# Kernel tuning notes

Hardware: AMD Instinct MI355X
Metric: run time of the kernel (lower is better)

Reference implementation:

```python
import jax, jax.numpy as jnp
import numpy as np

DIM = 512
KEY_DIM = 32
NUM_HEADS = 8
ATTN_RATIO = 4
RES = 1024
B = 16
NH_KD = KEY_DIM * NUM_HEADS          # 256
D = ATTN_RATIO * KEY_DIM             # 128
DH = D * NUM_HEADS                   # 1024
H_QKV = DH + 2 * NH_KD               # 1536
EPS = 1e-5
SCALE = KEY_DIM ** -0.5


def bn(y, g, b, m, v):
    # eval-mode BatchNorm1d over channel dim of [B, C, L]
    inv = g / jnp.sqrt(v + EPS)
    return (y - m[None, :, None]) * inv[None, :, None] + b[None, :, None]


def setup_inputs() -> dict:
    key = jax.random.key(0)
    ks = jax.random.split(key, 16)
    x = jax.random.normal(ks[0], (B, DIM, RES), dtype=jnp.float32)
    w_qkv = jax.random.normal(ks[1], (H_QKV, DIM), dtype=jnp.float32) * 0.02
    qkv_g = jnp.ones((H_QKV,), jnp.float32)
    qkv_b = jnp.zeros((H_QKV,), jnp.float32)
    qkv_m = jax.random.normal(ks[2], (H_QKV,), jnp.float32) * 0.1
    qkv_v = jax.random.uniform(ks[3], (H_QKV,), jnp.float32) + 0.5
    w_dw = jax.random.normal(ks[4], (NH_KD, 1, 3), jnp.float32) * 0.1
    dw_g = jnp.ones((NH_KD,), jnp.float32)
    dw_b = jnp.zeros((NH_KD,), jnp.float32)
    dw_m = jax.random.normal(ks[5], (NH_KD,), jnp.float32) * 0.1
    dw_v = jax.random.uniform(ks[6], (NH_KD,), jnp.float32) + 0.5
    w_proj = jax.random.normal(ks[7], (DIM, DH), jnp.float32) * 0.02
    proj_g = jnp.ones((DIM,), jnp.float32)  # bn_weight_init=0 in source, use 1 for nontrivial output
    proj_b = jnp.zeros((DIM,), jnp.float32)
    proj_m = jax.random.normal(ks[8], (DIM,), jnp.float32) * 0.1
    proj_v = jax.random.uniform(ks[9], (DIM,), jnp.float32) + 0.5
    attention_biases = jax.random.normal(ks[10], (NUM_HEADS, RES), jnp.float32) * 0.02
    pts = jnp.arange(RES)
    bias_idxs = jnp.abs(pts[:, None] - pts[None, :]).astype(jnp.int32)  # [N, N]
    return dict(x=x, w_qkv=w_qkv, qkv_g=qkv_g, qkv_b=qkv_b, qkv_m=qkv_m, qkv_v=qkv_v,
                w_dw=w_dw, dw_g=dw_g, dw_b=dw_b, dw_m=dw_m, dw_v=dw_v,
                w_proj=w_proj, proj_g=proj_g, proj_b=proj_b, proj_m=proj_m, proj_v=proj_v,
                attention_biases=attention_biases, bias_idxs=bias_idxs)


def reference(x, w_qkv, qkv_g, qkv_b, qkv_m, qkv_v,
              w_dw, dw_g, dw_b, dw_m, dw_v,
              w_proj, proj_g, proj_b, proj_m, proj_v,
              attention_biases, bias_idxs):
    Bsz, _, L = x.shape
    # qkv: conv1x1 + BN
    qkv = bn(jnp.einsum('bcl,oc->bol', x, w_qkv), qkv_g, qkv_b, qkv_m, qkv_v)
    q = qkv[:, :NH_KD]
    k = qkv[:, NH_KD:2 * NH_KD]
    v = qkv[:, 2 * NH_KD:]
    # depthwise conv k=3 pad=1 on q, then BN
    q = jax.lax.conv_general_dilated(q, w_dw, window_strides=(1,), padding=((1, 1),),
                                     dimension_numbers=('NCH', 'OIH', 'NCH'),
                                     feature_group_count=NH_KD)
    q = bn(q, dw_g, dw_b, dw_m, dw_v)
    q = q.reshape(Bsz, NUM_HEADS, KEY_DIM, L)
    k = k.reshape(Bsz, NUM_HEADS, KEY_DIM, L)
    v = v.reshape(Bsz, NUM_HEADS, D, L)
    ab = attention_biases[:, bias_idxs]  # [H, N, N]
    attn = jnp.einsum('bhdn,bhdm->bhnm', q, k) * SCALE + ab[None]
    attn = jax.nn.softmax(attn, axis=-1)
    out = jnp.einsum('bhdm,bhnm->bhdn', v, attn).reshape(Bsz, DH, L)
    # proj: ReLU -> conv1x1 -> BN
    out = jax.nn.relu(out)
    out = bn(jnp.einsum('bcl,oc->bol', out, w_proj), proj_g, proj_b, proj_m, proj_v)
    return out
```

## Files before the change

### kernel.cpp

```cpp
#include <hip/hip_runtime.h>
#include <stdint.h>

#define DEV __device__ __forceinline__

typedef unsigned short u16;
typedef __bf16 bf16x8 __attribute__((ext_vector_type(8)));
typedef float floatx4 __attribute__((ext_vector_type(4)));
typedef unsigned short u16x4 __attribute__((ext_vector_type(4)));
typedef unsigned short u16x8 __attribute__((ext_vector_type(8)));
typedef short s16x4 __attribute__((ext_vector_type(4)));


DEV u16 f2bf(float x) {
  union { float f; uint32_t u; } v; v.f = x;
  uint32_t r = v.u + 0x7FFFu + ((v.u >> 16) & 1u);
  return (u16)(r >> 16);
}
DEV float bf2f(u16 x) {
  union { uint32_t u; float f; } v; v.u = ((uint32_t)x) << 16;
  return v.f;
}
DEV float loadf(const void* p, int i, int bf) {
  return bf ? bf2f(((const u16*)p)[i]) : ((const float*)p)[i];
}
DEV u16 fastbf(float x) {
  union { float f; uint32_t u; } v; v.f = x;
  return (u16)((v.u + 0x8000u) >> 16);
}
DEV bf16x8 u2b(u16x8 v) {
  union { u16x8 u; bf16x8 b; } x; x.u = v; return x.b;
}

DEV floatx4 mfma16(bf16x8 a, bf16x8 b, floatx4 c) {
  return __builtin_amdgcn_mfma_f32_16x16x32_bf16(a, b, c, 0, 0, 0);
}

DEV void gl_lds16(const void* g, void* l) {
  __builtin_amdgcn_global_load_lds(
      (const __attribute__((address_space(1))) void*)g,
      (__attribute__((address_space(3))) void*)l, 16, 0, 0);
}

__global__ void sniff(const uint32_t* __restrict__ x, int* __restrict__ flag) {
  int lane = threadIdx.x & 63;
  int hits = 0;
#pragma unroll
  for (int i = 0; i < 4; ++i) {
    uint32_t u = x[lane * 4 + i];
    int e = (u >> 7) & 0xFF;
    hits += (e >= 100 && e <= 140) ? 1 : 0;
  }
  unsigned long long m = __ballot(hits >= 3);
  if (lane == 0) *flag = (__popcll(m) >= 40) ? 1 : 0;
}

__global__ __launch_bounds__(256) void cvt_all(
    const void* __restrict__ a, const void* __restrict__ b,
    const void* __restrict__ c, const void* __restrict__ d,
    u16* __restrict__ oa, u16* __restrict__ ob, u16* __restrict__ oc,
    u16* __restrict__ od, const int* __restrict__ flag) {
  int i = blockIdx.x * 256 + threadIdx.x;
  int bf = *flag;
  if (i < 786432) {
    oa[i] = bf ? ((const u16*)a)[i] : f2bf(((const float*)a)[i]);
  } else if (i < 1310720) {
    int j = i - 786432;
    ob[j] = bf ? ((const u16*)b)[j] : f2bf(((const float*)b)[j]);
  } else if (i < 1311488) {
    int j = i - 1310720;
    oc[j] = bf ? ((const u16*)c)[j] : f2bf(((const float*)c)[j]);
  } else if (i < 1319680) {
    int j = i - 1311488;
    od[j] = bf ? ((const u16*)d)[j] : f2bf(((const float*)d)[j]);
  }
}

__global__ __launch_bounds__(256) void prep_params(
    const void* qg, const void* qb, const void* qm, const void* qv,
    const void* dg, const void* db, const void* dm, const void* dv,
    const void* pg, const void* pb, const void* pm, const void* pv,
    float* scl, float* shf, const int* __restrict__ flag) {
  int i = blockIdx.x * 256 + threadIdx.x;
  if (i >= 2304) return;
  int bf = *flag;
  float g, b, m, v;
  if (i < 1536)      { g = loadf(qg, i, bf); b = loadf(qb, i, bf); m = loadf(qm, i, bf); v = loadf(qv, i, bf); }
  else if (i < 1792) { int j = i - 1536; g = loadf(dg, j, bf); b = loadf(db, j, bf); m = loadf(dm, j, bf); v = loadf(dv, j, bf); }
  else               { int j = i - 1792; g = loadf(pg, j, bf); b = loadf(pb, j, bf); m = loadf(pm, j, bf); v = loadf(pv, j, bf); }
  float s = g / sqrtf(v + 1e-5f);
  scl[i] = s;
  shf[i] = b - m * s;
}

__global__ __launch_bounds__(256) void transpose_x(const void* __restrict__ x,
                                                   u16* __restrict__ xT,
                                                   const int* __restrict__ flag) {
  __shared__ __align__(16) u16 tile[64 * 72];
  const int tid = threadIdx.x;
  const int b = blockIdx.z, c0 = blockIdx.y * 64, l0 = blockIdx.x * 64;
  const int bf = *flag;
  const size_t base = ((size_t)b * 512 + c0) * 1024 + l0;
  if (bf) {
    const u16* xb = (const u16*)x + base;
#pragma unroll
    for (int it = 0; it < 4; ++it) {
      int flat = it * 256 + tid;
      int row = flat >> 4, c4 = flat & 15;
      u16x4 v = *(const u16x4*)(xb + (size_t)row * 1024 + c4 * 4);
      tile[(c4 * 4 + 0) * 72 + row] = v.x;
      tile[(c4 * 4 + 1) * 72 + row] = v.y;
      tile[(c4 * 4 + 2) * 72 + row] = v.z;
      tile[(c4 * 4 + 3) * 72 + row] = v.w;
    }
  } else {
    const float* xb = (const float*)x + base;
#pragma unroll
    for (int it = 0; it < 4; ++it) {
      int flat = it * 256 + tid;
      int row = flat >> 4, c4 = flat & 15;
      floatx4 v = *(const floatx4*)(xb + (size_t)row * 1024 + c4 * 4);
      tile[(c4 * 4 + 0) * 72 + row] = f2bf(v[0]);
      tile[(c4 * 4 + 1) * 72 + row] = f2bf(v[1]);
      tile[(c4 * 4 + 2) * 72 + row] = f2bf(v[2]);
      tile[(c4 * 4 + 3) * 72 + row] = f2bf(v[3]);
    }
  }
  __syncthreads();
  u16* xTb = xT + ((size_t)b * 1024 + l0) * 512 + c0;
#pragma unroll
  for (int it = 0; it < 4; ++it) {
    int flat = it * 256 + tid;
    int row = flat >> 4, c4 = flat & 15;
    u16x4 v = *(const u16x4*)&tile[row * 72 + c4 * 4];
    *(u16x4*)(xTb + (size_t)row * 512 + c4 * 4) = v;
  }
}

template <int K>
__global__ __launch_bounds__(256) void gemm_bn(
    const u16* __restrict__ A, const u16* __restrict__ BT, u16* __restrict__ Y,
    const float* __restrict__ scl, const float* __restrict__ shf, int sclOff,
    const int* __restrict__ flag, int outFlagged) {
  __shared__ __align__(16) u16 lds[4 * 64 * 72];
  const int tid = threadIdx.x, lane = tid & 63, w = tid >> 6;
  const int l15 = lane & 15, quad = lane >> 4;
  const int o_blk = blockIdx.y * 128, l_blk = blockIdx.x * 128, b = blockIdx.z;
  const int o_off = (w >> 1) * 64, l_off = (w & 1) * 64;
  const u16* BTb = BT + (size_t)b * 1024 * K;

  floatx4 acc[4][4];
#pragma unroll
  for (int i = 0; i < 4; ++i)
#pragma unroll
    for (int j = 0; j < 4; ++j) acc[i][j] = (floatx4){0.f, 0.f, 0.f, 0.f};

  for (int k0 = 0; k0 < K; k0 += 32) {
    __syncthreads();
#pragma unroll
    for (int s = 0; s < 2; ++s) {
      const int chunk = (s * 4 + w) * 1024;
      const int byteoff = chunk + lane * 16;
      const int row = byteoff >> 6;
      const int col = (byteoff & 63) >> 1;
      gl_lds16(A + (size_t)(o_blk + row) * K + k0 + col, &lds[chunk >> 1]);
      gl_lds16(BTb + (size_t)(l_blk + row) * K + k0 + col, &lds[4096 + (chunk >> 1)]);
    }
    __syncthreads();
    bf16x8 af[4], bfr[4];
#pragma unroll
    for (int ir = 0; ir < 4; ++ir)
      af[ir] = *(const bf16x8*)&lds[(o_off + 16 * ir + l15) * 32 + quad * 8];
#pragma unroll
    for (int jc = 0; jc < 4; ++jc)
      bfr[jc] = *(const bf16x8*)&lds[4096 + (l_off + 16 * jc + l15) * 32 + quad * 8];
#pragma unroll
    for (int ir = 0; ir < 4; ++ir)
#pragma unroll
      for (int jc = 0; jc < 4; ++jc)
        acc[ir][jc] = mfma16(af[ir], bfr[jc], acc[ir][jc]);
  }
  __syncthreads();
  u16* eb = &lds[w * 4608];
#pragma unroll
  for (int ir = 0; ir < 4; ++ir) {
#pragma unroll
    for (int r = 0; r < 4; ++r) {
      int rloc = 16 * ir + quad * 4 + r;
      int o = o_blk + o_off + rloc;
      float s = scl[sclOff + o], hh = shf[sclOff + o];
#pragma unroll
      for (int jc = 0; jc < 4; ++jc)
        eb[rloc * 72 + 16 * jc + l15] = f2bf(acc[ir][jc][r] * s + hh);
    }
  }
  asm volatile("s_waitcnt lgkmcnt(0)" ::: "memory");
  const int M = gridDim.y * 128;
  const size_t ybase = ((size_t)b * M + o_blk + o_off) * 1024 + l_blk + l_off;
  const int outbf = outFlagged ? *flag : 1;
  if (outbf) {
#pragma unroll
    for (int it = 0; it < 8; ++it) {
      int flat = it * 64 + lane;
      int row = flat >> 3, g = flat & 7;
      u16x8 v = *(const u16x8*)&eb[row * 72 + g * 8];
      *(u16x8*)(Y + ybase + (size_t)row * 1024 + g * 8) = v;
    }
  } else {
    float* Yf = (float*)Y;
#pragma unroll
    for (int it = 0; it < 8; ++it) {
      int flat = it * 64 + lane;
      int row = flat >> 3, g = flat & 7;
      u16x8 v = *(const u16x8*)&eb[row * 72 + g * 8];
      floatx4 lo, hi;
#pragma unroll
      for (int t = 0; t < 4; ++t) { lo[t] = bf2f(v[t]); hi[t] = bf2f(v[4 + t]); }
      *(floatx4*)(Yf + ybase + (size_t)row * 1024 + g * 8) = lo;
      *(floatx4*)(Yf + ybase + (size_t)row * 1024 + g * 8 + 4) = hi;
    }
  }
}

__global__ __launch_bounds__(256) void dwconv_pack(
    const u16* __restrict__ qkv, const u16* __restrict__ w_dw,
    const float* __restrict__ scl, const float* __restrict__ shf,
    u16* __restrict__ qT, u16* __restrict__ kT) {
  __shared__ __align__(16) u16 lds[256 * 36];
  const int tid = threadIdx.x;
  const int lch = blockIdx.x, h = blockIdx.y, b = blockIdx.z;
  const int r = tid >> 3, seg = tid & 7;
  const int l0 = lch * 256 + seg * 32;
  {
    const int o = h * 32 + r;
    const u16* base = qkv + ((size_t)b * 1536 + o) * 1024;
    float w0 = bf2f(w_dw[o * 3 + 0]), w1 = bf2f(w_dw[o * 3 + 1]), w2 = bf2f(w_dw[o * 3 + 2]);
    float sc = scl[1536 + o], sh = shf[1536 + o];
    float prev = (l0 > 0) ? bf2f(base[l0 - 1]) : 0.f;
    float cur = bf2f(base[l0]);
#pragma unroll 4
    for (int j = 0; j < 32; ++j) {
      int lg = l0 + j;
      float nxt = (lg + 1 < 1024) ? bf2f(base[lg + 1]) : 0.f;
      lds[(seg * 32 + j) * 36 + r] = f2bf((w0 * prev + w1 * cur + w2 * nxt) * sc + sh);
      prev = cur; cur = nxt;
    }
  }
  __syncthreads();
  {
    const size_t qTb = (((size_t)b * 8 + h) * 1024 + lch * 256) * 32;
#pragma unroll
    for (int it = 0; it < 8; ++it) {
      int flat = it * 256 + tid;
      int ll = flat >> 3, g = flat & 7;
      u16x4 v = *(const u16x4*)&lds[ll * 36 + g * 4];
      *(u16x4*)(qT + qTb + (size_t)ll * 32 + g * 4) = v;
    }
  }
  __syncthreads();
  {
    const int o = 256 + h * 32 + r;
    const u16* base = qkv + ((size_t)b * 1536 + o) * 1024;
#pragma unroll 8
    for (int j = 0; j < 32; ++j) lds[(seg * 32 + j) * 36 + r] = base[l0 + j];
  }
  __syncthreads();
  {
    const size_t kTb = (((size_t)b * 8 + h) * 1024 + lch * 256) * 32;
#pragma unroll
    for (int it = 0; it < 8; ++it) {
      int flat = it * 256 + tid;
      int ll = flat >> 3, g = flat & 7;
      u16x4 v = *(const u16x4*)&lds[ll * 36 + g * 4];
      *(u16x4*)(kT + kTb + (size_t)ll * 32 + g * 4) = v;
    }
  }
}

__global__ __launch_bounds__(512, 4) void attn(
    const u16* __restrict__ qT, const u16* __restrict__ kT,
    const u16* __restrict__ qkv, const u16* __restrict__ ab,
    u16* __restrict__ OT) {
  __shared__ __align__(16) float biasE[2048];
  __shared__ __align__(16) u16 ldsV[2 * 4096];
  const int tid = threadIdx.x, lane = tid & 63, w = tid >> 6;
  const int l15 = lane & 15, quad = lane >> 4;
  const int id = blockIdx.x;
  const int pair = id & 127, nb = id >> 7;
  const int b = pair >> 3, h = pair & 7;
  for (int i = tid; i < 2048; i += 512) {
    int dd = i - 1024;
    int idx = dd < 0 ? -dd : dd;
    if (idx > 1023) idx = 1023;
    biasE[i] = bf2f(ab[h * 1024 + idx]) * 1.44269504088896340f;
  }
  const int n0 = nb * 128 + w * 16;
  const size_t bh = ((size_t)b * 8 + h) * 1024;
  const u16* kTb = kT + bh * 32;
  const u16* vb = qkv + ((size_t)b * 1536 + 512 + h * 128) * 1024;
  const bf16x8 qf = *(const bf16x8*)(qT + bh * 32 + (size_t)(n0 + l15) * 32 + quad * 8);
  const int prow = 8 * (l15 >> 2) + (l15 & 3);
  const u16* kfp0 = kTb + (size_t)prow * 32 + quad * 8;
  const u16* kfp1 = kfp0 + 4 * 32;
  const int sd = tid >> 2, sc = tid & 3;
  const u16* sg = vb + (size_t)sd * 1024 + sc * 8;
  const int wv = (sd >> 4) * 512 + (sc * 16 + (sd & 15)) * 8;
  const int vrd = quad * 128 + l15 * 8;

  floatx4 oacc[8];
#pragma unroll
  for (int j = 0; j < 8; ++j) oacc[j] = (floatx4){0.f, 0.f, 0.f, 0.f};
  float rs = 0.f;
  constexpr float c1 = 0.17677669529663689f * 1.44269504088896340f;
  const floatx4 zf = (floatx4){0.f, 0.f, 0.f, 0.f};

  bf16x8 kc0 = *(const bf16x8*)(kfp0);
  bf16x8 kc1 = *(const bf16x8*)(kfp1);
  {
    u16x8 a = *(const u16x8*)sg;
    *(u16x8*)&ldsV[wv] = a;
  }
  __syncthreads();

#pragma unroll 1
  for (int m0 = 0; m0 < 1024; m0 += 32) {
    const int par = (m0 >> 5) & 1;
    const bool more = (m0 + 32) < 1024;
    u16x8 a;
    bf16x8 kn0, kn1;
    if (more) {
      a = *(const u16x8*)(sg + m0 + 32);
      kn0 = *(const bf16x8*)(kfp0 + (size_t)(m0 + 32) * 32);
      kn1 = *(const bf16x8*)(kfp1 + (size_t)(m0 + 32) * 32);
    }
    floatx4 s0 = mfma16(kc0, qf, zf);
    floatx4 s1 = mfma16(kc1, qf, zf);
    const int Cb = 1024 + n0 + l15 - 8 * quad - m0;
    u16x8 pf;
#pragma unroll
    for (int r = 0; r < 4; ++r) {
      float p0 = __builtin_amdgcn_exp2f(s0[r] * c1 + biasE[Cb - r]);
      float p1 = __builtin_amdgcn_exp2f(s1[r] * c1 + biasE[Cb - 4 - r]);
      rs += p0 + p1;
      pf[r] = fastbf(p0);
      pf[4 + r] = fastbf(p1);
    }
    const bf16x8 pfb = u2b(pf);
    const int rbase = par * 4096 + vrd;
#pragma unroll
    for (int jd = 0; jd < 8; ++jd) {
      bf16x8 vv = *(const bf16x8*)&ldsV[rbase + jd * 512];
      oacc[jd] = mfma16(vv, pfb, oacc[jd]);
    }
    if (more) {
      *(u16x8*)&ldsV[(par ^ 1) * 4096 + wv] = a;
      kc0 = kn0;
      kc1 = kn1;
    }
    __syncthreads();
  }
  rs += __shfl_xor(rs, 16, 64);
  rs += __shfl_xor(rs, 32, 64);
  const float inv = __builtin_amdgcn_rcpf(rs);
  u16* OTb = OT + ((size_t)b * 1024 + n0 + l15) * 1024 + h * 128 + quad * 4;
#pragma unroll
  for (int jd = 0; jd < 8; ++jd) {
    u16x4 o;
#pragma unroll
    for (int r = 0; r < 4; ++r) {
      float v = oacc[jd][r] * inv;
      o[r] = fastbf(v > 0.f ? v : 0.f);
    }
    *(u16x4*)(OTb + 16 * jd) = o;
  }
}

extern "C" void kernel_launch(void* const* d_in, const int* in_sizes, int n_in,
                              void* d_out, int out_size, void* d_ws, size_t ws_size,
                              hipStream_t stream) {
  const void* x      = d_in[0];
  const void* w_qkv  = d_in[1];
  const void* qkv_g  = d_in[2];
  const void* qkv_b  = d_in[3];
  const void* qkv_m  = d_in[4];
  const void* qkv_v  = d_in[5];
  const void* w_dw   = d_in[6];
  const void* dw_g   = d_in[7];
  const void* dw_b   = d_in[8];
  const void* dw_m   = d_in[9];
  const void* dw_v   = d_in[10];
  const void* w_proj = d_in[11];
  const void* proj_g = d_in[12];
  const void* proj_b = d_in[13];
  const void* proj_m = d_in[14];
  const void* proj_v = d_in[15];
  const void* abias  = d_in[16];

  char* ws = (char*)d_ws;
  u16*   xT      = (u16*)(ws);
  u16*   qkv     = (u16*)(ws + 16777216);
  u16*   qT      = (u16*)(ws + 67108864);
  u16*   kT      = (u16*)(ws + 75497472);
  u16*   OT      = (u16*)(ws + 83886080);
  float* scl     = (float*)(ws + 117440512);
  float* shf     = (float*)(ws + 117449728);
  u16*   wqkv_c  = (u16*)(ws + 117458944);
  u16*   wproj_c = (u16*)(ws + 119031808);
  u16*   wdw_c   = (u16*)(ws + 120080384);
  u16*   ab_c    = (u16*)(ws + 120082432);
  int*   flag    = (int*)(ws + 120098816);
  if (ws_size < (size_t)120098880) return;

  sniff<<<1, 64, 0, stream>>>((const uint32_t*)x, flag);
  cvt_all<<<5155, 256, 0, stream>>>(w_qkv, w_proj, w_dw, abias,
                                    wqkv_c, wproj_c, wdw_c, ab_c, flag);
  prep_params<<<9, 256, 0, stream>>>(qkv_g, qkv_b, qkv_m, qkv_v, dw_g, dw_b, dw_m,
                                     dw_v, proj_g, proj_b, proj_m, proj_v, scl, shf, flag);
  transpose_x<<<dim3(16, 8, 16), 256, 0, stream>>>(x, xT, flag);
  gemm_bn<512><<<dim3(8, 12, 16), 256, 0, stream>>>(wqkv_c, xT, qkv, scl, shf, 0, flag, 0);
  dwconv_pack<<<dim3(4, 8, 16), 256, 0, stream>>>(qkv, wdw_c, scl, shf, qT, kT);
  attn<<<1024, 512, 0, stream>>>(qT, kT, qkv, ab_c, OT);
  gemm_bn<1024><<<dim3(8, 4, 16), 256, 0, stream>>>(wproj_c, OT, (u16*)d_out, scl, shf, 1792, flag, 1);
}
```

Before: 270.6 us.

## Load V fragments directly from global memory instead of LDS double buffer

Removes the shared-memory double buffer for V and the per-iteration block barrier. Each wave now reads its V fragments straight from global memory (through L2/L1) into registers before the MFMAs, and the K prefetch for the next step is folded in. This drops the LDS staging traffic and the syncs, but every one of the 8 waves now fetches the same V tile redundantly from cache. Load latency is also only partly hidden, since the loads are issued at the top of the same iteration that uses them.

```diff
diff --git a/kernel.cpp b/kernel.cpp
--- a/kernel.cpp
+++ b/kernel.cpp
@@ -281,7 +281,6 @@
     const u16* __restrict__ qkv, const u16* __restrict__ ab,
     u16* __restrict__ OT) {
   __shared__ __align__(16) float biasE[2048];
-  __shared__ __align__(16) u16 ldsV[2 * 4096];
   const int tid = threadIdx.x, lane = tid & 63, w = tid >> 6;
   const int l15 = lane & 15, quad = lane >> 4;
   const int id = blockIdx.x;
@@ -301,10 +300,7 @@
   const int prow = 8 * (l15 >> 2) + (l15 & 3);
   const u16* kfp0 = kTb + (size_t)prow * 32 + quad * 8;
   const u16* kfp1 = kfp0 + 4 * 32;
-  const int sd = tid >> 2, sc = tid & 3;
-  const u16* sg = vb + (size_t)sd * 1024 + sc * 8;
-  const int wv = (sd >> 4) * 512 + (sc * 16 + (sd & 15)) * 8;
-  const int vrd = quad * 128 + l15 * 8;
+  const u16* vrow = vb + (size_t)l15 * 1024 + 8 * quad;
 
   floatx4 oacc[8];
 #pragma unroll
@@ -315,25 +311,21 @@
 
   bf16x8 kc0 = *(const bf16x8*)(kfp0);
   bf16x8 kc1 = *(const bf16x8*)(kfp1);
-  {
-    u16x8 a = *(const u16x8*)sg;
-    *(u16x8*)&ldsV[wv] = a;
-  }
   __syncthreads();
 
 #pragma unroll 1
   for (int m0 = 0; m0 < 1024; m0 += 32) {
-    const int par = (m0 >> 5) & 1;
-    const bool more = (m0 + 32) < 1024;
-    u16x8 a;
-    bf16x8 kn0, kn1;
-    if (more) {
-      a = *(const u16x8*)(sg + m0 + 32);
-      kn0 = *(const bf16x8*)(kfp0 + (size_t)(m0 + 32) * 32);
-      kn1 = *(const bf16x8*)(kfp1 + (size_t)(m0 + 32) * 32);
-    }
+    bf16x8 vv[8];
+#pragma unroll
+    for (int jd = 0; jd < 8; ++jd)
+      vv[jd] = *(const bf16x8*)(vrow + jd * 16384 + m0);
     floatx4 s0 = mfma16(kc0, qf, zf);
     floatx4 s1 = mfma16(kc1, qf, zf);
+    const bool more = (m0 + 32) < 1024;
+    if (more) {
+      kc0 = *(const bf16x8*)(kfp0 + (size_t)(m0 + 32) * 32);
+      kc1 = *(const bf16x8*)(kfp1 + (size_t)(m0 + 32) * 32);
+    }
     const int Cb = 1024 + n0 + l15 - 8 * quad - m0;
     u16x8 pf;
 #pragma unroll
@@ -345,18 +337,9 @@
       pf[4 + r] = fastbf(p1);
     }
     const bf16x8 pfb = u2b(pf);
-    const int rbase = par * 4096 + vrd;
-#pragma unroll
-    for (int jd = 0; jd < 8; ++jd) {
-      bf16x8 vv = *(const bf16x8*)&ldsV[rbase + jd * 512];
-      oacc[jd] = mfma16(vv, pfb, oacc[jd]);
-    }
-    if (more) {
-      *(u16x8*)&ldsV[(par ^ 1) * 4096 + wv] = a;
-      kc0 = kn0;
-      kc1 = kn1;
-    }
-    __syncthreads();
+#pragma unroll
+    for (int jd = 0; jd < 8; ++jd)
+      oacc[jd] = mfma16(vv[jd], pfb, oacc[jd]);
   }
   rs += __shfl_xor(rs, 16, 64);
   rs += __shfl_xor(rs, 32, 64);
```

After: 458.7 us. 69.5% more time.
